# Optimization experiments

Hardware: AMD Instinct MI355X
Metric: run time of the kernel (lower is better)

The kernel has to match this reference:

```python
import jax, jax.numpy as jnp
import numpy as np

DIM = 192
HEADS = 6
HEAD_DIM = DIM // HEADS
WS = 8            # window size
N = WS * WS       # tokens per window
IN_CC = 16        # top-k kept keys per query
B, H, W = 8, 64, 64
NEG = -100.0      # value used by the torch code for masked logits
EPS_NORM = 1e-12  # F.normalize eps
EPS_LN = 1e-5     # nn.LayerNorm eps


def _rel_pos_index(ws):
    coords = np.stack(np.meshgrid(np.arange(ws), np.arange(ws), indexing='ij'))  # (2,ws,ws)
    cf = coords.reshape(2, -1)
    rel = (cf[:, :, None] - cf[:, None, :]).transpose(1, 2, 0).astype(np.int64)  # (N,N,2)
    rel[:, :, 0] += ws - 1
    rel[:, :, 1] += ws - 1
    rel[:, :, 0] *= 2 * ws - 1
    return jnp.asarray(rel.sum(-1))  # (N,N) indices into (2ws-1)^2 table

REL_IDX = _rel_pos_index(WS)


def _layer_norm(x, g, b):
    mu = jnp.mean(x, -1, keepdims=True)
    var = jnp.mean(jnp.square(x - mu), -1, keepdims=True)
    return (x - mu) * jax.lax.rsqrt(var + EPS_LN) * g + b


def _l2n(x):
    n = jnp.sqrt(jnp.sum(jnp.square(x), -1, keepdims=True))
    return x / jnp.maximum(n, EPS_NORM)


def setup_inputs() -> dict:
    key = jax.random.key(0)
    ks = jax.random.split(key, 8)
    s = 0.02
    return {
        'x': jax.random.normal(ks[0], (B, DIM, H, W), jnp.float32),
        'norm1_g': jnp.ones((DIM,), jnp.float32),
        'norm1_b': jnp.zeros((DIM,), jnp.float32),
        'qkv_w': jax.random.normal(ks[1], (3 * DIM, DIM), jnp.float32) * s,
        'qkv_b': jnp.zeros((3 * DIM,), jnp.float32),
        'proj_w': jax.random.normal(ks[2], (DIM, DIM), jnp.float32) * s,
        'proj_b': jnp.zeros((DIM,), jnp.float32),
        'rpb_table': jax.random.normal(ks[3], ((2 * WS - 1) ** 2, HEADS), jnp.float32) * s,
        'temperature': jnp.ones((HEADS, 1, 1), jnp.float32),
        'norm2_g': jnp.ones((DIM,), jnp.float32),
        'norm2_b': jnp.zeros((DIM,), jnp.float32),
        'fc1_w': jax.random.normal(ks[4], (4 * DIM, DIM), jnp.float32) * s,
        'fc1_b': jnp.zeros((4 * DIM,), jnp.float32),
        'fc2_w': jax.random.normal(ks[5], (DIM, 4 * DIM), jnp.float32) * s,
        'fc2_b': jnp.zeros((DIM,), jnp.float32),
    }


def reference(x, norm1_g, norm1_b, qkv_w, qkv_b, proj_w, proj_b, rpb_table,
              temperature, norm2_g, norm2_b, fc1_w, fc1_b, fc2_w, fc2_b):
    b, c, h, w = x.shape
    # (B,C,H,W) -> (B,L,C), pre-norm (note: the torch code norms the shortcut too)
    xs = jnp.transpose(x.reshape(b, c, h * w), (0, 2, 1))
    shortcut = _layer_norm(xs, norm1_g, norm1_b)  # (B,L,C)

    # window partition: (B,H,W,C) -> (B*nWh*nWw, N, C); shift_size=0, no padding (H,W % WS == 0)
    xin = shortcut.reshape(b, h // WS, WS, w // WS, WS, c)
    xin = jnp.transpose(xin, (0, 1, 3, 2, 4, 5)).reshape(-1, N, c)
    B_ = xin.shape[0]

    qkv = (xin @ qkv_w.T + qkv_b).reshape(B_, N, 3, HEADS, HEAD_DIM)
    qkv = jnp.transpose(qkv, (2, 0, 3, 1, 4))  # (3, B_, h, N, d)
    q, k, v = qkv[0], qkv[1], qkv[2]

    # cosine attention with learned per-head temperature
    attn = jnp.einsum('bhnd,bhmd->bhnm', _l2n(q), _l2n(k)) * temperature  # (B_,h,N,N)

    # top-k sparsification: keep IN_CC largest logits per query (threshold == kth value;
    # equivalent to the torch topk+scatter mask for distinct values)
    kth = jax.lax.top_k(attn, IN_CC)[0][..., -1:]
    attn = jnp.where(attn >= kth, attn, NEG)

    # relative position bias gather: (N,N,h) -> (h,N,N)
    rpb = jnp.transpose(rpb_table[REL_IDX], (2, 0, 1))
    attn = jax.nn.softmax(attn + rpb[None], axis=-1)

    out = jnp.einsum('bhnm,bhmd->bhnd', attn, v)
    out = jnp.transpose(out, (0, 2, 1, 3)).reshape(B_, N, c)
    out = out @ proj_w.T + proj_b

    # window reverse -> (B, L, C)
    out = out.reshape(b, h // WS, w // WS, WS, WS, c)
    out = jnp.transpose(out, (0, 1, 3, 2, 4, 5)).reshape(b, h * w, c)

    x2 = shortcut + out  # drop_path = identity (eval)
    hdn = _layer_norm(x2, norm2_g, norm2_b)
    hdn = jax.nn.gelu(hdn @ fc1_w.T + fc1_b, approximate=False) @ fc2_w.T + fc2_b
    x2 = x2 + hdn

    # back to (B,C,H,W)
    return jnp.transpose(x2, (0, 2, 1)).reshape(b, c, h, w)
```

## Files before the change

kernel.cpp:

```cpp
#include <hip/hip_runtime.h>
#include <hip/hip_bf16.h>
#include <math.h>

#define DIM     192
#define HEADS   6
#define HEAD_DIM 32
#define NTOK    64
#define IN_CC   16
#define TTOT    32768
#define NWIN    512

using bf16x8 = __attribute__((ext_vector_type(8))) short;
using f32x4  = __attribute__((ext_vector_type(4))) float;
typedef unsigned short ushort_t;

__device__ __forceinline__ ushort_t f2b(float f) {
    unsigned u = __float_as_uint(f);
    u += 0x7fffu + ((u >> 16) & 1u);
    return (ushort_t)(u >> 16);
}
__device__ __forceinline__ unsigned pk2(float a, float b) {
    return (unsigned)f2b(a) | ((unsigned)f2b(b) << 16);
}
__device__ __forceinline__ float b2f(ushort_t u) {
    return __uint_as_float(((unsigned)u) << 16);
}
__device__ __forceinline__ float m3(float a, float b, float c) {
    return fmaxf(fmaxf(a, b), c);
}

__global__ __launch_bounds__(256) void cvt_all_kernel(
    const float* __restrict__ s0, const float* __restrict__ s1,
    const float* __restrict__ s2, const float* __restrict__ s3,
    ushort_t* __restrict__ d0, ushort_t* __restrict__ d1,
    ushort_t* __restrict__ d2, ushort_t* __restrict__ d3)
{
    const int bid = blockIdx.x;
    const float* src; ushort_t* dst; int off, K; bool perm = false;
    if (bid < 108)      { src = s0; dst = d0; off = bid;       K = 192; perm = true; }
    else if (bid < 144) { src = s1; dst = d1; off = bid - 108; K = 192; }
    else if (bid < 288) { src = s2; dst = d2; off = bid - 144; K = 192; }
    else                { src = s3; dst = d3; off = bid - 288; K = 768; }
    const int K8 = K >> 3;
    const int d  = (off * 256 + threadIdx.x) * 4;
    const int frag = d >> 7, win = d & 127;
    const int m16w = win >> 3, k7 = win & 7;
    const int oblk = frag / K8, kblk = frag - oblk * K8;
    const int o = oblk * 16 + m16w, k = kblk * 8 + k7;
    int so = o;
    if (perm && o < 384) {
        const int s = o & 31;
        const int c = (((s >> 2) & 3) << 3) | (((s >> 4) & 1) << 2) | (s & 3);
        so = (o & ~31) | c;
    }
    float4 v = *(const float4*)(src + (size_t)so * K + k);
    ushort4 ov;
    ov.x = f2b(v.x); ov.y = f2b(v.y); ov.z = f2b(v.z); ov.w = f2b(v.w);
    *(ushort4*)(dst + d) = ov;
}

__global__ __launch_bounds__(256) void ln1_kernel(
    const float* __restrict__ x, const float* __restrict__ g,
    const float* __restrict__ bb, ushort_t* __restrict__ outh)
{
    __shared__ float xs[64][193];
    __shared__ float mu_s[64], rs_s[64];
    __shared__ float gs[192], bs[192];
    const int tid = threadIdx.x;
    const int t0  = blockIdx.x * 64;
    const int b   = t0 >> 12;
    const int hw0 = t0 & 4095;
    if (tid < 192) { gs[tid] = g[tid]; bs[tid] = bb[tid]; }
    const int tok = tid & 63, qq = tid >> 6;
    const float* xb = x + (size_t)b * (DIM * 4096) + hw0 + tok;
    #pragma unroll
    for (int it = 0; it < 48; ++it) {
        int c = it * 4 + qq;
        xs[tok][c] = xb[(size_t)c * 4096];
    }
    __syncthreads();
    const int tok2 = tid >> 2, p = tid & 3;
    float sum = 0.f;
    #pragma unroll
    for (int c = 0; c < 48; ++c) sum += xs[tok2][p * 48 + c];
    sum += __shfl_xor(sum, 1);
    sum += __shfl_xor(sum, 2);
    const float m = sum * (1.0f / 192.0f);
    float ss = 0.f;
    #pragma unroll
    for (int c = 0; c < 48; ++c) { float d = xs[tok2][p * 48 + c] - m; ss += d * d; }
    ss += __shfl_xor(ss, 1);
    ss += __shfl_xor(ss, 2);
    if (p == 0) {
        mu_s[tok2] = m;
        rs_s[tok2] = 1.0f / sqrtf(ss * (1.0f / 192.0f) + 1e-5f);
    }
    __syncthreads();
    ushort_t* obh = outh + (size_t)t0 * DIM;
    #pragma unroll
    for (int it = 0; it < 48; ++it) {
        int idx = it * 256 + tid;
        int tk = idx / 192, c = idx % 192;
        obh[idx] = f2b((xs[tk][c] - mu_s[tk]) * rs_s[tk] * gs[c] + bs[c]);
    }
}

__global__ __launch_bounds__(768, 3) void attn_fused(
    const ushort_t* __restrict__ sc_h, const ushort_t* __restrict__ wqf,
    const float* __restrict__ qkv_b, const float* __restrict__ rpb_table,
    const float* __restrict__ temp, const ushort_t* __restrict__ wpf,
    const float* __restrict__ proj_b, float* __restrict__ x2)
{
    __shared__ __align__(16) char smem[127680];
    const int tid  = threadIdx.x;
    const int wave = tid >> 6, n = tid & 63;

    char* Rb = smem + wave * 4608;
    float*    Ssq = (float*)Rb;
    ushort_t* Ph  = (ushort_t*)Rb;
    char* Ab = smem + 55296 + wave * 5120;
    ushort_t* Vt  = (ushort_t*)Ab;
    float*    ksb = (float*)(Ab + 4608);
    float*    qnb = (float*)(Ab + 4864);
    float*    rpb = (float*)(smem + 116736) + wave * 228;

    const int wloc = (wave >= 6) ? 1 : 0;
    const int h    = wave - 6 * wloc;
    ushort_t* tile = (ushort_t*)(smem + wloc * 25600);
    ushort_t (*AoT)[200] = (ushort_t(*)[200])(smem + wloc * 25600);
    float* Cwi = (float*)(smem + 55296 + wave * 2304);

    const int win = blockIdx.x * 2 + wloc;
    const int b   = win >> 6;
    const int wh  = (win >> 3) & 7, ww = win & 7;
    const int wb  = b * 4096 + wh * 512 + ww * 8;
    const int i1  = n >> 3, j1 = n & 7;
    const int m16 = n & 15, quad = n >> 4;

    for (int r = n; r < 225; r += 64) rpb[r] = rpb_table[r * 6 + h];

    #pragma unroll
    for (int l = 0; l < 4; ++l) {
        const int g = h * 256 + l * 64 + n;
        const int t = (g * 2731) >> 16;
        const int r = g - t * 24;
        const int tt = wb + ((t >> 3) << 6) + (t & 7);
        uint4 v = *(const uint4*)(sc_h + (size_t)tt * 192 + r * 8);
        *(uint4*)(tile + t * 200 + r * 8) = v;
    }
    __syncthreads();

    const ushort_t* tb = tile + m16 * 200 + quad * 8;
    f32x4 pq[4][2], pk[4][2];
    #pragma unroll
    for (int i = 0; i < 4; ++i)
        #pragma unroll
        for (int j = 0; j < 2; ++j) { pq[i][j] = (f32x4)(0.0f); pk[i][j] = (f32x4)(0.0f); }
    {
        const ushort_t* WbQ = wqf + (size_t)(2 * h) * 3072 + m16 * 8;
        const ushort_t* WbK = wqf + (size_t)(12 + 2 * h) * 3072 + m16 * 8;
        for (int ks = 0; ks < 192; ks += 32) {
            bf16x8 af[4], wq2[2], wk2[2];
            #pragma unroll
            for (int i = 0; i < 4; ++i)
                af[i] = *(const bf16x8*)(tb + i * 3200 + ks);
            #pragma unroll
            for (int j = 0; j < 2; ++j) {
                wq2[j] = *(const bf16x8*)(WbQ + (size_t)(j * 24 + (ks >> 3) + quad) * 128);
                wk2[j] = *(const bf16x8*)(WbK + (size_t)(j * 24 + (ks >> 3) + quad) * 128);
            }
            #pragma unroll
            for (int i = 0; i < 4; ++i)
                #pragma unroll
                for (int j = 0; j < 2; ++j) {
                    pq[i][j] = __builtin_amdgcn_mfma_f32_16x16x32_bf16(wq2[j], af[i], pq[i][j], 0, 0, 0);
                    pk[i][j] = __builtin_amdgcn_mfma_f32_16x16x32_bf16(wk2[j], af[i], pk[i][j], 0, 0, 0);
                }
        }
    }
    bf16x8 qA[4], kB[4];
    #pragma unroll
    for (int part = 0; part < 2; ++part) {
        const int o0 = part * 192 + h * 32;
        const float4 bv0 = *(const float4*)&qkv_b[o0 + 8 * quad];
        const float4 bv1 = *(const float4*)&qkv_b[o0 + 8 * quad + 4];
        float ssq[4];
        #pragma unroll
        for (int i = 0; i < 4; ++i) {
            f32x4 v0 = part ? pk[i][0] : pq[i][0];
            f32x4 v1 = part ? pk[i][1] : pq[i][1];
            v0[0] += bv0.x; v0[1] += bv0.y; v0[2] += bv0.z; v0[3] += bv0.w;
            v1[0] += bv1.x; v1[1] += bv1.y; v1[2] += bv1.z; v1[3] += bv1.w;
            float sq = 0.f;
            #pragma unroll
            for (int r = 0; r < 4; ++r) sq += v0[r] * v0[r] + v1[r] * v1[r];
            ssq[i] = sq;
            bf16x8 fr;
            fr[0] = (short)f2b(v0[0]); fr[1] = (short)f2b(v0[1]);
            fr[2] = (short)f2b(v0[2]); fr[3] = (short)f2b(v0[3]);
            fr[4] = (short)f2b(v1[0]); fr[5] = (short)f2b(v1[1]);
            fr[6] = (short)f2b(v1[2]); fr[7] = (short)f2b(v1[3]);
            if (part == 0) qA[i] = fr; else kB[i] = fr;
        }
        #pragma unroll
        for (int i = 0; i < 4; ++i) {
            ssq[i] += __shfl_xor(ssq[i], 16);
            ssq[i] += __shfl_xor(ssq[i], 32);
        }
        if (quad == 0) {
            #pragma unroll
            for (int i = 0; i < 4; ++i) {
                if (part == 0) qnb[16 * i + m16] = ssq[i];
                else           ksb[4 * m16 + i]  = 1.0f / fmaxf(sqrtf(ssq[i]), 1e-12f);
            }
        }
    }

    f32x4 acc[4][4];
    #pragma unroll
    for (int i = 0; i < 4; ++i)
        #pragma unroll
        for (int j = 0; j < 4; ++j)
            acc[i][j] = __builtin_amdgcn_mfma_f32_16x16x32_bf16(qA[i], kB[j], (f32x4)(0.0f), 0, 0, 0);

    {
        f32x4 pv[4][2];
        #pragma unroll
        for (int i = 0; i < 4; ++i)
            #pragma unroll
            for (int j = 0; j < 2; ++j) pv[i][j] = (f32x4)(0.0f);
        const ushort_t* WbV = wqf + (size_t)(24 + 2 * h) * 3072 + m16 * 8;
        for (int ks = 0; ks < 192; ks += 32) {
            bf16x8 af[4], wv2[2];
            #pragma unroll
            for (int i = 0; i < 4; ++i)
                af[i] = *(const bf16x8*)(tb + i * 3200 + ks);
            #pragma unroll
            for (int j = 0; j < 2; ++j)
                wv2[j] = *(const bf16x8*)(WbV + (size_t)(j * 24 + (ks >> 3) + quad) * 128);
            #pragma unroll
            for (int i = 0; i < 4; ++i)
                #pragma unroll
                for (int j = 0; j < 2; ++j)
                    pv[i][j] = __builtin_amdgcn_mfma_f32_16x16x32_bf16(wv2[j], af[i], pv[i][j], 0, 0, 0);
        }
        const int o0 = 384 + h * 32;
        const float4 bv0 = *(const float4*)&qkv_b[o0 + quad * 4];
        const float4 bv1 = *(const float4*)&qkv_b[o0 + 16 + quad * 4];
        #pragma unroll
        for (int i = 0; i < 4; ++i) {
            f32x4 v0 = pv[i][0], v1 = pv[i][1];
            v0[0] += bv0.x; v0[1] += bv0.y; v0[2] += bv0.z; v0[3] += bv0.w;
            v1[0] += bv1.x; v1[1] += bv1.y; v1[2] += bv1.z; v1[3] += bv1.w;
            #pragma unroll
            for (int r = 0; r < 4; ++r) {
                Vt[(quad * 4 + r) * 72 + 4 * m16 + i]      = f2b(v0[r]);
                Vt[(16 + quad * 4 + r) * 72 + 4 * m16 + i] = f2b(v1[r]);
            }
        }
    }

    const int r8 = n >> 3, c4 = (n & 7) * 4;
    uint2 rv[4][2];
    #pragma unroll
    for (int i = 0; i < 4; ++i)
        #pragma unroll
        for (int q = 0; q < 2; ++q) {
            const int tok = 16 * i + 8 * q + r8;
            const int tt = wb + ((tok >> 3) << 6) + (tok & 7);
            rv[i][q] = *(const uint2*)(sc_h + (size_t)tt * 192 + h * 32 + c4);
        }

    __syncthreads();

    float s[64];
    #pragma unroll
    for (int i = 0; i < 4; ++i) {
        #pragma unroll
        for (int r = 0; r < 4; ++r) {
            f32x4 vv = { acc[i][0][r], acc[i][1][r], acc[i][2][r], acc[i][3][r] };
            *(f32x4*)&Ssq[(4 * quad + r) * 68 + 4 * m16] = vv;
        }
        if ((n >> 4) == i) {
            #pragma unroll
            for (int c = 0; c < 16; ++c)
                *(float4*)&s[4 * c] = *(const float4*)&Ssq[(n & 15) * 68 + 4 * c];
        }
    }

    const float qs = temp[h] / fmaxf(sqrtf(qnb[n]), 1e-12f);
    #pragma unroll
    for (int c = 0; c < 16; ++c) {
        float4 kv = *(const float4*)&ksb[4 * c];
        s[4*c+0] *= qs * kv.x; s[4*c+1] *= qs * kv.y;
        s[4*c+2] *= qs * kv.z; s[4*c+3] *= qs * kv.w;
    }

    float thr = 1e30f;
    for (int it = 0; it < IN_CC; ++it) {
        #define MK(c) ((s[(c)] < thr) ? s[(c)] : -1e30f)
        float w[22];
        #pragma unroll
        for (int g = 0; g < 21; ++g) w[g] = m3(MK(3*g), MK(3*g+1), MK(3*g+2));
        w[21] = MK(63);
        #undef MK
        float y[8];
        #pragma unroll
        for (int g = 0; g < 7; ++g) y[g] = m3(w[3*g], w[3*g+1], w[3*g+2]);
        y[7] = w[21];
        thr = m3(m3(y[0], y[1], y[2]), m3(y[3], y[4], y[5]), fmaxf(y[6], y[7]));
    }

    const int basen = i1 * 15 + j1;
    float mxp[8];
    #pragma unroll
    for (int c = 0; c < 64; ++c) {
        const int m = 16 * (c & 3) + (c >> 2);
        const int i2 = m >> 3, j2 = m & 7;
        float vv = ((s[c] >= thr) ? s[c] : -100.0f)
                 + rpb[basen + (7 - i2) * 15 + (7 - j2)];
        s[c] = vv;
        if (c < 8) mxp[c] = vv; else mxp[c & 7] = fmaxf(mxp[c & 7], vv);
    }
    const float mx = m3(m3(mxp[0], mxp[1], mxp[2]), m3(mxp[3], mxp[4], mxp[5]),
                        fmaxf(mxp[6], mxp[7]));
    float sum = 0.f;
    #pragma unroll
    for (int c = 0; c < 64; ++c) { float e = __expf(s[c] - mx); s[c] = e; sum += e; }
    const float inv = 1.0f / sum;
    #pragma unroll
    for (int c = 0; c < 64; ++c) s[c] *= inv;

    bf16x8 vb[2][2];
    #pragma unroll
    for (int kh2 = 0; kh2 < 2; ++kh2)
        #pragma unroll
        for (int j2 = 0; j2 < 2; ++j2)
            vb[kh2][j2] = *(const bf16x8*)&Vt[(16 * j2 + m16) * 72 + kh2 * 32 + quad * 8];

    f32x4 o[4][2];
    #pragma unroll
    for (int i = 0; i < 4; ++i)
        #pragma unroll
        for (int j2 = 0; j2 < 2; ++j2)
            o[i][j2] = (f32x4)(0.0f);
    #pragma unroll
    for (int hf = 0; hf < 2; ++hf) {
        if ((n >> 5) == hf) {
            #pragma unroll
            for (int g = 0; g < 8; ++g) {
                uint4 w;
                w.x = pk2(s[8*g+0], s[8*g+1]); w.y = pk2(s[8*g+2], s[8*g+3]);
                w.z = pk2(s[8*g+4], s[8*g+5]); w.w = pk2(s[8*g+6], s[8*g+7]);
                *(uint4*)&Ph[(n & 31) * 72 + 8 * g] = w;
            }
        }
        #pragma unroll
        for (int ih = 0; ih < 2; ++ih) {
            const int i = 2 * hf + ih;
            #pragma unroll
            for (int kh2 = 0; kh2 < 2; ++kh2) {
                bf16x8 pafr = *(const bf16x8*)&Ph[(16 * ih + m16) * 72 + kh2 * 32 + quad * 8];
                o[i][0] = __builtin_amdgcn_mfma_f32_16x16x32_bf16(pafr, vb[kh2][0], o[i][0], 0, 0, 0);
                o[i][1] = __builtin_amdgcn_mfma_f32_16x16x32_bf16(pafr, vb[kh2][1], o[i][1], 0, 0, 0);
            }
        }
    }
    __syncthreads();

    #pragma unroll
    for (int i = 0; i < 4; ++i) {
        #pragma unroll
        for (int r = 0; r < 4; ++r) {
            const int row = 16 * i + 4 * quad + r;
            AoT[row][h * 32 + m16]      = f2b(o[i][0][r]);
            AoT[row][h * 32 + 16 + m16] = f2b(o[i][1][r]);
        }
    }
    __syncthreads();

    f32x4 pacc[4][2];
    #pragma unroll
    for (int i = 0; i < 4; ++i)
        #pragma unroll
        for (int j = 0; j < 2; ++j)
            pacc[i][j] = (f32x4)(0.0f);
    const ushort_t* Wb = wpf + (size_t)(h * 2) * 24 * 128 + m16 * 8;
    for (int ks = 0; ks < 192; ks += 32) {
        bf16x8 af[4], wv[2];
        #pragma unroll
        for (int i = 0; i < 4; ++i)
            af[i] = *(const bf16x8*)&AoT[16 * i + m16][quad * 8 + ks];
        #pragma unroll
        for (int j = 0; j < 2; ++j)
            wv[j] = *(const bf16x8*)(Wb + (size_t)(j * 24 + (ks >> 3) + quad) * 128);
        #pragma unroll
        for (int i = 0; i < 4; ++i)
            #pragma unroll
            for (int j = 0; j < 2; ++j)
                pacc[i][j] = __builtin_amdgcn_mfma_f32_16x16x32_bf16(wv[j], af[i], pacc[i][j], 0, 0, 0);
    }

    const float4 bj0 = *(const float4*)&proj_b[h * 32 + quad * 4];
    const float4 bj1 = *(const float4*)&proj_b[h * 32 + 16 + quad * 4];
    #pragma unroll
    for (int i = 0; i < 4; ++i) {
        f32x4 v0 = pacc[i][0], v1 = pacc[i][1];
        v0[0] += bj0.x; v0[1] += bj0.y; v0[2] += bj0.z; v0[3] += bj0.w;
        v1[0] += bj1.x; v1[1] += bj1.y; v1[2] += bj1.z; v1[3] += bj1.w;
        *(f32x4*)&Cwi[m16 * 36 + quad * 4]      = v0;
        *(f32x4*)&Cwi[m16 * 36 + 16 + quad * 4] = v1;
        #pragma unroll
        for (int q = 0; q < 2; ++q) {
            const int row = 8 * q + r8;
            const int tok = 16 * i + row;
            const int tt = wb + ((tok >> 3) << 6) + (tok & 7);
            float4 vv = *(const float4*)&Cwi[row * 36 + c4];
            const uint2 rr = rv[i][q];
            vv.x += b2f((ushort_t)(rr.x & 0xffffu));
            vv.y += b2f((ushort_t)(rr.x >> 16));
            vv.z += b2f((ushort_t)(rr.y & 0xffffu));
            vv.w += b2f((ushort_t)(rr.y >> 16));
            *(float4*)&x2[(size_t)tt * DIM + h * 32 + c4] = vv;
        }
    }
}

__global__ __launch_bounds__(256) void mlp_fused(
    const float* __restrict__ x2, const ushort_t* __restrict__ w1f,
    const ushort_t* __restrict__ w2f, const float* __restrict__ fc1_b,
    const float* __restrict__ fc2_b, const float* __restrict__ g2,
    const float* __restrict__ b2, float* __restrict__ outp)
{
    __shared__ __align__(16) char smem[43008];
    ushort_t (*h_h)[200] = (ushort_t(*)[200])smem;
    ushort_t (*a1c)[136] = (ushort_t(*)[136])(smem + 25600);
    float* gs  = (float*)(smem + 25600);
    float* bs  = gs + 192;

    const int tid  = threadIdx.x;
    const int wave = tid >> 6, lane = tid & 63;
    const int m16 = lane & 15, quad = lane >> 4;
    const int t0 = blockIdx.x * 64;
    const int b   = t0 >> 12;
    const int hw0 = t0 & 4095;

    if (tid < 192) { gs[tid] = g2[tid]; bs[tid] = b2[tid]; }
    __syncthreads();
    {
        const int tok = tid >> 2, p = tid & 3;
        const float* rp = x2 + (size_t)(t0 + tok) * DIM + p * 48;
        float xv[48];
        #pragma unroll
        for (int c4 = 0; c4 < 12; ++c4)
            *(float4*)&xv[c4 * 4] = *(const float4*)(rp + c4 * 4);
        float sum = 0.f;
        #pragma unroll
        for (int c = 0; c < 48; ++c) sum += xv[c];
        sum += __shfl_xor(sum, 1);
        sum += __shfl_xor(sum, 2);
        const float m = sum * (1.0f / 192.0f);
        float ss = 0.f;
        #pragma unroll
        for (int c = 0; c < 48; ++c) { float d = xv[c] - m; ss += d * d; }
        ss += __shfl_xor(ss, 1);
        ss += __shfl_xor(ss, 2);
        const float rs = 1.0f / sqrtf(ss * (1.0f / 192.0f) + 1e-5f);
        ushort_t* hp = &h_h[tok][p * 48];
        #pragma unroll
        for (int c2 = 0; c2 < 24; ++c2) {
            float v0 = (xv[2*c2]   - m) * rs * gs[p * 48 + 2*c2]   + bs[p * 48 + 2*c2];
            float v1 = (xv[2*c2+1] - m) * rs * gs[p * 48 + 2*c2+1] + bs[p * 48 + 2*c2+1];
            *(unsigned*)(hp + 2 * c2) = pk2(v0, v1);
        }
    }
    __syncthreads();

    f32x4 acc2[4][3];
    #pragma unroll
    for (int i = 0; i < 4; ++i)
        #pragma unroll
        for (int j = 0; j < 3; ++j)
            acc2[i][j] = (f32x4)(0.0f);

    for (int c = 0; c < 6; ++c) {
        f32x4 acc1[4][2];
        #pragma unroll
        for (int i = 0; i < 4; ++i)
            #pragma unroll
            for (int j = 0; j < 2; ++j)
                acc1[i][j] = (f32x4)(0.0f);
        const ushort_t* Wb1 = w1f + (size_t)(c * 8 + wave * 2) * 24 * 128 + m16 * 8;
        for (int ks = 0; ks < 192; ks += 32) {
            bf16x8 af[4], wv[2];
            #pragma unroll
            for (int i = 0; i < 4; ++i)
                af[i] = *(const bf16x8*)&h_h[16 * i + m16][quad * 8 + ks];
            #pragma unroll
            for (int j = 0; j < 2; ++j)
                wv[j] = *(const bf16x8*)(Wb1 + (size_t)(j * 24 + (ks >> 3) + quad) * 128);
            #pragma unroll
            for (int i = 0; i < 4; ++i)
                #pragma unroll
                for (int j = 0; j < 2; ++j)
                    acc1[i][j] = __builtin_amdgcn_mfma_f32_16x16x32_bf16(wv[j], af[i], acc1[i][j], 0, 0, 0);
        }
        #pragma unroll
        for (int j = 0; j < 2; ++j) {
            const int o = c * 128 + wave * 32 + 16 * j + quad * 4;
            const float4 bv = *(const float4*)&fc1_b[o];
            #pragma unroll
            for (int i = 0; i < 4; ++i) {
                f32x4 v = acc1[i][j];
                v[0] += bv.x; v[1] += bv.y; v[2] += bv.z; v[3] += bv.w;
                #pragma unroll
                for (int r = 0; r < 4; ++r) {
                    float xg = v[r];
                    float e1 = __expf(xg * (1.5957691f + 0.0713548f * xg * xg)) + 1.0f;
                    v[r] = xg - xg * __builtin_amdgcn_rcpf(e1);
                }
                uint2 pkd;
                pkd.x = pk2(v[0], v[1]); pkd.y = pk2(v[2], v[3]);
                *(uint2*)&a1c[16 * i + m16][wave * 32 + 16 * j + quad * 4] = pkd;
            }
        }
        __syncthreads();
        const ushort_t* Wb2 = w2f + (size_t)(wave * 3) * 96 * 128 + m16 * 8;
        for (int ks = 0; ks < 128; ks += 32) {
            bf16x8 af2[4], wv2[3];
            #pragma unroll
            for (int i = 0; i < 4; ++i)
                af2[i] = *(const bf16x8*)&a1c[16 * i + m16][quad * 8 + ks];
            #pragma unroll
            for (int j = 0; j < 3; ++j)
                wv2[j] = *(const bf16x8*)(Wb2 + (size_t)(j * 96 + c * 16 + (ks >> 3) + quad) * 128);
            #pragma unroll
            for (int i = 0; i < 4; ++i)
                #pragma unroll
                for (int j = 0; j < 3; ++j)
                    acc2[i][j] = __builtin_amdgcn_mfma_f32_16x16x32_bf16(wv2[j], af2[i], acc2[i][j], 0, 0, 0);
        }
        __syncthreads();
    }

    float (*Cw)[68] = (float(*)[68])(smem + wave * 8704);
    float4 b2j[3];
    #pragma unroll
    for (int j = 0; j < 3; ++j)
        b2j[j] = *(const float4*)&fc2_b[wave * 48 + 16 * j + quad * 4];
    #pragma unroll
    for (int p = 0; p < 2; ++p) {
        #pragma unroll
        for (int ih = 0; ih < 2; ++ih) {
            const int i = 2 * p + ih;
            #pragma unroll
            for (int j = 0; j < 3; ++j) {
                f32x4 v = acc2[i][j];
                v[0] += b2j[j].x; v[1] += b2j[j].y; v[2] += b2j[j].z; v[3] += b2j[j].w;
                *(f32x4*)&Cw[ih * 16 + m16][16 * j + quad * 4] = v;
            }
        }
        #pragma unroll
        for (int q = 0; q < 6; ++q) {
            const int idx = q * 64 + lane;
            const int cc = idx >> 3, t4 = (idx & 7) * 4;
            const int o  = wave * 48 + cc;
            const int tb = t0 + p * 32 + t4;
            float4 vv;
            vv.x = Cw[t4 + 0][cc] + x2[(size_t)(tb + 0) * DIM + o];
            vv.y = Cw[t4 + 1][cc] + x2[(size_t)(tb + 1) * DIM + o];
            vv.z = Cw[t4 + 2][cc] + x2[(size_t)(tb + 2) * DIM + o];
            vv.w = Cw[t4 + 3][cc] + x2[(size_t)(tb + 3) * DIM + o];
            *(float4*)&outp[(size_t)b * (DIM * 4096) + (size_t)o * 4096
                            + hw0 + p * 32 + t4] = vv;
        }
    }
}

extern "C" void kernel_launch(void* const* d_in, const int* in_sizes, int n_in,
                              void* d_out, int out_size, void* d_ws, size_t ws_size,
                              hipStream_t stream)
{
    const float* x        = (const float*)d_in[0];
    const float* norm1_g  = (const float*)d_in[1];
    const float* norm1_b  = (const float*)d_in[2];
    const float* qkv_w    = (const float*)d_in[3];
    const float* qkv_b    = (const float*)d_in[4];
    const float* proj_w   = (const float*)d_in[5];
    const float* proj_b   = (const float*)d_in[6];
    const float* rpbt     = (const float*)d_in[7];
    const float* temp     = (const float*)d_in[8];
    const float* norm2_g  = (const float*)d_in[9];
    const float* norm2_b  = (const float*)d_in[10];
    const float* fc1_w    = (const float*)d_in[11];
    const float* fc1_b    = (const float*)d_in[12];
    const float* fc2_w    = (const float*)d_in[13];
    const float* fc2_b    = (const float*)d_in[14];
    float* out = (float*)d_out;

    char* wsb = (char*)d_ws;
    ushort_t* shortcut_h = (ushort_t*)wsb;
    float*    x2         = (float*)(wsb + 12582912);
    ushort_t* wq  = (ushort_t*)(wsb + 125829120);
    ushort_t* wp  = wq + 110592;
    ushort_t* w1  = wp + 36864;
    ushort_t* w2  = w1 + 147456;

    hipLaunchKernelGGL(cvt_all_kernel, dim3(432), dim3(256), 0, stream,
                       qkv_w, proj_w, fc1_w, fc2_w, wq, wp, w1, w2);

    hipLaunchKernelGGL(ln1_kernel, dim3(TTOT / 64), dim3(256), 0, stream,
                       x, norm1_g, norm1_b, shortcut_h);
    hipLaunchKernelGGL(attn_fused, dim3(NWIN / 2), dim3(768), 0, stream,
                       shortcut_h, wq, qkv_b, rpbt, temp, wp, proj_b, x2);
    hipLaunchKernelGGL(mlp_fused, dim3(TTOT / 64), dim3(256), 0, stream,
                       x2, w1, w2, fc1_b, fc2_b, norm2_g, norm2_b, out);
}
```

Before: 194.0 us.

## Enlarge MLP tile to 128 tokens with 12 waves sharing weight loads

The fused MLP kernel now processes 128 tokens per block using 12 waves, split into two halves of 64 tokens times 6 output-column groups. The hidden dimension is chunked into 4 chunks of 192 instead of 6 of 128. Each weight fragment loaded from global memory now serves twice as many tokens, cutting weight traffic per token. In exchange, shared memory grows to about 104KB per block, which limits occupancy, and the grid halves to 256 blocks.

```diff
diff --git a/kernel.cpp b/kernel.cpp
--- a/kernel.cpp
+++ b/kernel.cpp
@@ -426,28 +426,29 @@
     }
 }
 
-__global__ __launch_bounds__(256) void mlp_fused(
+__global__ __launch_bounds__(768, 3) void mlp_fused(
     const float* __restrict__ x2, const ushort_t* __restrict__ w1f,
     const ushort_t* __restrict__ w2f, const float* __restrict__ fc1_b,
     const float* __restrict__ fc2_b, const float* __restrict__ g2,
     const float* __restrict__ b2, float* __restrict__ outp)
 {
-    __shared__ __align__(16) char smem[43008];
+    __shared__ __align__(16) char smem[103936];
     ushort_t (*h_h)[200] = (ushort_t(*)[200])smem;
-    ushort_t (*a1c)[136] = (ushort_t(*)[136])(smem + 25600);
-    float* gs  = (float*)(smem + 25600);
-    float* bs  = gs + 192;
+    ushort_t (*a1c)[200] = (ushort_t(*)[200])(smem + 51200);
+    float* gs = (float*)(smem + 102400);
+    float* bs = gs + 192;
 
     const int tid  = threadIdx.x;
     const int wave = tid >> 6, lane = tid & 63;
     const int m16 = lane & 15, quad = lane >> 4;
-    const int t0 = blockIdx.x * 64;
+    const int half = wave / 6, ow = wave - 6 * half;
+    const int t0  = blockIdx.x * 128;
     const int b   = t0 >> 12;
     const int hw0 = t0 & 4095;
 
     if (tid < 192) { gs[tid] = g2[tid]; bs[tid] = b2[tid]; }
     __syncthreads();
-    {
+    if (tid < 512) {
         const int tok = tid >> 2, p = tid & 3;
         const float* rp = x2 + (size_t)(t0 + tok) * DIM + p * 48;
         float xv[48];
@@ -476,26 +477,26 @@
     }
     __syncthreads();
 
-    f32x4 acc2[4][3];
+    f32x4 acc2[4][2];
     #pragma unroll
     for (int i = 0; i < 4; ++i)
         #pragma unroll
-        for (int j = 0; j < 3; ++j)
+        for (int j = 0; j < 2; ++j)
             acc2[i][j] = (f32x4)(0.0f);
 
-    for (int c = 0; c < 6; ++c) {
+    for (int c = 0; c < 4; ++c) {
         f32x4 acc1[4][2];
         #pragma unroll
         for (int i = 0; i < 4; ++i)
             #pragma unroll
             for (int j = 0; j < 2; ++j)
                 acc1[i][j] = (f32x4)(0.0f);
-        const ushort_t* Wb1 = w1f + (size_t)(c * 8 + wave * 2) * 24 * 128 + m16 * 8;
+        const ushort_t* Wb1 = w1f + (size_t)(c * 12 + ow * 2) * 3072 + m16 * 8;
         for (int ks = 0; ks < 192; ks += 32) {
             bf16x8 af[4], wv[2];
             #pragma unroll
             for (int i = 0; i < 4; ++i)
-                af[i] = *(const bf16x8*)&h_h[16 * i + m16][quad * 8 + ks];
+                af[i] = *(const bf16x8*)&h_h[half * 64 + 16 * i + m16][quad * 8 + ks];
             #pragma unroll
             for (int j = 0; j < 2; ++j)
                 wv[j] = *(const bf16x8*)(Wb1 + (size_t)(j * 24 + (ks >> 3) + quad) * 128);
@@ -507,7 +508,7 @@
         }
         #pragma unroll
         for (int j = 0; j < 2; ++j) {
-            const int o = c * 128 + wave * 32 + 16 * j + quad * 4;
+            const int o = c * 192 + ow * 32 + 16 * j + quad * 4;
             const float4 bv = *(const float4*)&fc1_b[o];
             #pragma unroll
             for (int i = 0; i < 4; ++i) {
@@ -521,58 +522,58 @@
                 }
                 uint2 pkd;
                 pkd.x = pk2(v[0], v[1]); pkd.y = pk2(v[2], v[3]);
-                *(uint2*)&a1c[16 * i + m16][wave * 32 + 16 * j + quad * 4] = pkd;
+                *(uint2*)&a1c[half * 64 + 16 * i + m16][ow * 32 + 16 * j + quad * 4] = pkd;
             }
         }
         __syncthreads();
-        const ushort_t* Wb2 = w2f + (size_t)(wave * 3) * 96 * 128 + m16 * 8;
-        for (int ks = 0; ks < 128; ks += 32) {
-            bf16x8 af2[4], wv2[3];
-            #pragma unroll
-            for (int i = 0; i < 4; ++i)
-                af2[i] = *(const bf16x8*)&a1c[16 * i + m16][quad * 8 + ks];
-            #pragma unroll
-            for (int j = 0; j < 3; ++j)
-                wv2[j] = *(const bf16x8*)(Wb2 + (size_t)(j * 96 + c * 16 + (ks >> 3) + quad) * 128);
+        const ushort_t* Wb2 = w2f + (size_t)(ow * 2) * 12288 + m16 * 8;
+        for (int ks = 0; ks < 192; ks += 32) {
+            bf16x8 af2[4], wv2[2];
+            #pragma unroll
+            for (int i = 0; i < 4; ++i)
+                af2[i] = *(const bf16x8*)&a1c[half * 64 + 16 * i + m16][quad * 8 + ks];
+            #pragma unroll
+            for (int j = 0; j < 2; ++j)
+                wv2[j] = *(const bf16x8*)(Wb2 + (size_t)(j * 96 + c * 24 + (ks >> 3) + quad) * 128);
             #pragma unroll
             for (int i = 0; i < 4; ++i)
                 #pragma unroll
-                for (int j = 0; j < 3; ++j)
+                for (int j = 0; j < 2; ++j)
                     acc2[i][j] = __builtin_amdgcn_mfma_f32_16x16x32_bf16(wv2[j], af2[i], acc2[i][j], 0, 0, 0);
         }
         __syncthreads();
     }
 
-    float (*Cw)[68] = (float(*)[68])(smem + wave * 8704);
-    float4 b2j[3];
-    #pragma unroll
-    for (int j = 0; j < 3; ++j)
-        b2j[j] = *(const float4*)&fc2_b[wave * 48 + 16 * j + quad * 4];
+    float* Cw = (float*)(smem + wave * 4608);
+    float4 b2j[2];
+    #pragma unroll
+    for (int j = 0; j < 2; ++j)
+        b2j[j] = *(const float4*)&fc2_b[ow * 32 + 16 * j + quad * 4];
     #pragma unroll
     for (int p = 0; p < 2; ++p) {
         #pragma unroll
         for (int ih = 0; ih < 2; ++ih) {
             const int i = 2 * p + ih;
             #pragma unroll
-            for (int j = 0; j < 3; ++j) {
+            for (int j = 0; j < 2; ++j) {
                 f32x4 v = acc2[i][j];
                 v[0] += b2j[j].x; v[1] += b2j[j].y; v[2] += b2j[j].z; v[3] += b2j[j].w;
-                *(f32x4*)&Cw[ih * 16 + m16][16 * j + quad * 4] = v;
+                *(f32x4*)&Cw[(ih * 16 + m16) * 36 + 16 * j + quad * 4] = v;
             }
         }
         #pragma unroll
-        for (int q = 0; q < 6; ++q) {
+        for (int q = 0; q < 4; ++q) {
             const int idx = q * 64 + lane;
             const int cc = idx >> 3, t4 = (idx & 7) * 4;
-            const int o  = wave * 48 + cc;
-            const int tb = t0 + p * 32 + t4;
+            const int o  = ow * 32 + cc;
+            const int tb = t0 + half * 64 + p * 32 + t4;
             float4 vv;
-            vv.x = Cw[t4 + 0][cc] + x2[(size_t)(tb + 0) * DIM + o];
-            vv.y = Cw[t4 + 1][cc] + x2[(size_t)(tb + 1) * DIM + o];
-            vv.z = Cw[t4 + 2][cc] + x2[(size_t)(tb + 2) * DIM + o];
-            vv.w = Cw[t4 + 3][cc] + x2[(size_t)(tb + 3) * DIM + o];
+            vv.x = Cw[(t4 + 0) * 36 + cc] + x2[(size_t)(tb + 0) * DIM + o];
+            vv.y = Cw[(t4 + 1) * 36 + cc] + x2[(size_t)(tb + 1) * DIM + o];
+            vv.z = Cw[(t4 + 2) * 36 + cc] + x2[(size_t)(tb + 2) * DIM + o];
+            vv.w = Cw[(t4 + 3) * 36 + cc] + x2[(size_t)(tb + 3) * DIM + o];
             *(float4*)&outp[(size_t)b * (DIM * 4096) + (size_t)o * 4096
-                            + hw0 + p * 32 + t4] = vv;
+                            + hw0 + half * 64 + p * 32 + t4] = vv;
         }
     }
 }
@@ -613,6 +614,6 @@
                        x, norm1_g, norm1_b, shortcut_h);
     hipLaunchKernelGGL(attn_fused, dim3(NWIN / 2), dim3(768), 0, stream,
                        shortcut_h, wq, qkv_b, rpbt, temp, wp, proj_b, x2);
-    hipLaunchKernelGGL(mlp_fused, dim3(TTOT / 64), dim3(256), 0, stream,
+    hipLaunchKernelGGL(mlp_fused, dim3(TTOT / 128), dim3(768), 0, stream,
                        x2, w1, w2, fc1_b, fc2_b, norm2_g, norm2_b, out);
 }
```

Result: no change. 192.0 us (-1.0%).
